# Kernel tuning notes

Hardware: AMD Instinct MI355X
Metric: run time of the kernel (lower is better)

Reference implementation:

```python
import jax, jax.numpy as jnp
import numpy as np

EMBED = 1024
HEADS = 16
HEAD_DIM = EMBED // HEADS


def setup_inputs() -> dict:
    key = jax.random.key(0)
    ks = jax.random.split(key, 11)
    B, S = 2, 2048
    scale = 1.0 / np.sqrt(EMBED)
    inp = {
        'Q': jax.random.normal(ks[0], (B, S, EMBED), jnp.float32),
        'K': jax.random.normal(ks[1], (B, S, EMBED), jnp.float32),
        'V': jax.random.normal(ks[2], (B, S, EMBED), jnp.float32),
        'Wq': jax.random.normal(ks[3], (EMBED, EMBED), jnp.float32) * scale,
        'bq': jnp.zeros((EMBED,), jnp.float32),
        'Wk': jax.random.normal(ks[4], (EMBED, EMBED), jnp.float32) * scale,
        'bk': jnp.zeros((EMBED,), jnp.float32),
        'Wv': jax.random.normal(ks[5], (EMBED, EMBED), jnp.float32) * scale,
        'bv': jnp.zeros((EMBED,), jnp.float32),
        'Wo': jax.random.normal(ks[6], (EMBED, EMBED), jnp.float32) * scale,
        'bo': jnp.zeros((EMBED,), jnp.float32),
    }
    return inp


def reference(Q, K, V, Wq, bq, Wk, bk, Wv, bv, Wo, bo):
    B, Sq, _ = Q.shape
    Sk = K.shape[1]
    # linear projections (torch nn.Linear: x @ W.T + b; here W stored as [in,out])
    q = Q @ Wq + bq
    k = K @ Wk + bk
    v = V @ Wv + bv
    # [B, H, S, D]
    q = q.reshape(B, Sq, HEADS, HEAD_DIM).transpose(0, 2, 1, 3)
    k = k.reshape(B, Sk, HEADS, HEAD_DIM).transpose(0, 2, 1, 3)
    v = v.reshape(B, Sk, HEADS, HEAD_DIM).transpose(0, 2, 1, 3)
    scores = jnp.einsum('bhqd,bhkd->bhqk', q, k) / jnp.sqrt(jnp.float32(HEAD_DIM))
    attn = jax.nn.softmax(scores, axis=-1)
    out = jnp.einsum('bhqk,bhkd->bhqd', attn, v)
    out = out.transpose(0, 2, 1, 3).reshape(B, Sq, EMBED)
    return out @ Wo + bo
```

## Files before the change

kernel.cpp:

```cpp
#include <hip/hip_runtime.h>

#define EMBED 1024
#define HEADS 16
#define HDIM  64
#define BATCH 2
#define SEQ   2048
#define MTOK  (BATCH*SEQ)

typedef _Float16 half_t;
typedef __attribute__((ext_vector_type(4))) float    f32x4;
typedef __attribute__((ext_vector_type(8))) _Float16 f16x8;
typedef __attribute__((ext_vector_type(4))) _Float16 f16x4;

#define MFMA16(a,b,c) __builtin_amdgcn_mfma_f32_16x16x32_f16(a,b,c,0,0,0)

#define GLOAD_LDS16(gp, lp)                                                     \
    __builtin_amdgcn_global_load_lds(                                           \
        (const __attribute__((address_space(1))) void*)(gp),                    \
        (__attribute__((address_space(3))) void*)(lp), 16, 0, 0)

#define QSCALE 0.18033688f

__global__ __launch_bounds__(256) void wt_kernel(const float* __restrict__ W0,
                                                 const float* __restrict__ W1,
                                                 const float* __restrict__ W2,
                                                 const float* __restrict__ W3,
                                                 half_t* __restrict__ T0,
                                                 half_t* __restrict__ T1,
                                                 half_t* __restrict__ T2,
                                                 half_t* __restrict__ T3)
{
    const int z = blockIdx.z;
    const float* W = (z == 0) ? W0 : (z == 1) ? W1 : (z == 2) ? W2 : W3;
    half_t* WT     = (z == 0) ? T0 : (z == 1) ? T1 : (z == 2) ? T2 : T3;

    __shared__ float tile[64][68];
    const int t  = threadIdx.x;
    const int n0 = blockIdx.x * 64;
    const int k0 = blockIdx.y * 64;
#pragma unroll
    for (int i = 0; i < 4; ++i) {
        int f = t + 256 * i;
        int r = f >> 4, c4 = (f & 15) << 2;
        float4 v = *(const float4*)(W + (size_t)(k0 + r) * EMBED + n0 + c4);
        tile[r][c4 + 0] = v.x; tile[r][c4 + 1] = v.y;
        tile[r][c4 + 2] = v.z; tile[r][c4 + 3] = v.w;
    }
    __syncthreads();
#pragma unroll
    for (int i = 0; i < 4; ++i) {
        int f = t + 256 * i;
        int nr = f >> 4, kc = (f & 15) << 2;
        f16x4 o;
        o[0] = (half_t)tile[kc + 0][nr];
        o[1] = (half_t)tile[kc + 1][nr];
        o[2] = (half_t)tile[kc + 2][nr];
        o[3] = (half_t)tile[kc + 3][nr];
        *(f16x4*)(WT + (size_t)(n0 + nr) * EMBED + k0 + kc) = o;
    }
}

__global__ __launch_bounds__(256, 3) void proj3_kernel(const float* __restrict__ Aq,
                                                       const float* __restrict__ Ak,
                                                       const float* __restrict__ Av,
                                                       const half_t* __restrict__ Btq,
                                                       const half_t* __restrict__ Btk,
                                                       const half_t* __restrict__ Btv,
                                                       const float*  __restrict__ bq,
                                                       const float*  __restrict__ bk,
                                                       const float*  __restrict__ bv,
                                                       half_t* __restrict__ oq,
                                                       half_t* __restrict__ ok,
                                                       half_t* __restrict__ ov)
{
    const int z = blockIdx.z;
    const float*  A    = (z == 0) ? Aq  : (z == 1) ? Ak  : Av;
    const half_t* Bt   = (z == 0) ? Btq : (z == 1) ? Btk : Btv;
    const float*  bias = (z == 0) ? bq  : (z == 1) ? bk  : bv;
    half_t*       out  = (z == 0) ? oq  : (z == 1) ? ok  : ov;

    __shared__ half_t As[128 * 64];
    __shared__ half_t Bs[128 * 64];
    const int tid = threadIdx.x, lane = tid & 63, g = lane >> 4, ln = lane & 15;
    const int w = tid >> 6, wm = w >> 1, wn = w & 1;
    const int m0 = blockIdx.x * 128, n0 = blockIdx.y * 128;
    const int srow8 = lane >> 3, schunk = lane & 7;

    f32x4 acc[4][4];
#pragma unroll
    for (int i = 0; i < 4; ++i)
#pragma unroll
        for (int j = 0; j < 4; ++j) acc[i][j] = (f32x4){0.f, 0.f, 0.f, 0.f};

    float4 v0[4], v1[4];
#pragma unroll
    for (int i = 0; i < 4; ++i) {
        int row = (i * 4 + w) * 8 + srow8;
        const float* src = A + (size_t)(m0 + row) * EMBED + schunk * 8;
        v0[i] = *(const float4*)(src);
        v1[i] = *(const float4*)(src + 4);
    }

    for (int kt = 0; kt < EMBED; kt += 64) {
#pragma unroll
        for (int i = 0; i < 4; ++i) {
            int row = (i * 4 + w) * 8 + srow8;
            GLOAD_LDS16(Bt + (size_t)(n0 + row) * EMBED + kt + schunk * 8,
                        (char*)Bs + (i * 4 + w) * 1024);
        }
#pragma unroll
        for (int i = 0; i < 4; ++i) {
            int row = (i * 4 + w) * 8 + srow8;
            f16x8 hv;
            hv[0] = (half_t)v0[i].x; hv[1] = (half_t)v0[i].y;
            hv[2] = (half_t)v0[i].z; hv[3] = (half_t)v0[i].w;
            hv[4] = (half_t)v1[i].x; hv[5] = (half_t)v1[i].y;
            hv[6] = (half_t)v1[i].z; hv[7] = (half_t)v1[i].w;
            *(f16x8*)(As + (size_t)row * 64 + schunk * 8) = hv;
        }
        __syncthreads();

        if (kt + 64 < EMBED) {
#pragma unroll
            for (int i = 0; i < 4; ++i) {
                int row = (i * 4 + w) * 8 + srow8;
                const float* src = A + (size_t)(m0 + row) * EMBED + kt + 64 + schunk * 8;
                v0[i] = *(const float4*)(src);
                v1[i] = *(const float4*)(src + 4);
            }
        }

#pragma unroll
        for (int k2 = 0; k2 < 2; ++k2) {
            f16x8 af[4], bf[4];
#pragma unroll
            for (int mi = 0; mi < 4; ++mi)
                af[mi] = *(const f16x8*)(As + (wm * 64 + mi * 16 + ln) * 64 + k2 * 32 + g * 8);
#pragma unroll
            for (int ni = 0; ni < 4; ++ni)
                bf[ni] = *(const f16x8*)(Bs + (wn * 64 + ni * 16 + ln) * 64 + k2 * 32 + g * 8);
#pragma unroll
            for (int mi = 0; mi < 4; ++mi)
#pragma unroll
                for (int ni = 0; ni < 4; ++ni)
                    acc[mi][ni] = MFMA16(af[mi], bf[ni], acc[mi][ni]);
        }
        __syncthreads();
    }

#pragma unroll
    for (int mi = 0; mi < 4; ++mi) {
#pragma unroll
        for (int ni = 0; ni < 4; ++ni) {
            int col = n0 + wn * 64 + ni * 16 + ln;
            float bb = bias[col];
            int h = col >> 6, d = col & 63;
            if (z == 2) {
                int row0 = m0 + wm * 64 + mi * 16 + g * 4;
                int b = row0 >> 11, s = row0 & 2047;
                f16x4 o4;
#pragma unroll
                for (int r = 0; r < 4; ++r)
                    o4[r] = (half_t)(acc[mi][ni][r] + bb);
                *(f16x4*)(out + ((size_t)(b * HEADS + h) * HDIM + d) * SEQ + s) = o4;
            } else {
#pragma unroll
                for (int r = 0; r < 4; ++r) {
                    int row = m0 + wm * 64 + mi * 16 + g * 4 + r;
                    int b = row >> 11, s = row & 2047;
                    float val = acc[mi][ni][r] + bb;
                    if (z == 0) val *= QSCALE;
                    out[((size_t)(b * HEADS + h) * SEQ + s) * HDIM + d] = (half_t)val;
                }
            }
        }
    }
}

__global__ __launch_bounds__(256, 4) void final_kernel(const half_t* __restrict__ A,
                                                       const half_t* __restrict__ Bt,
                                                       const float*  __restrict__ bias,
                                                       float* __restrict__ out)
{
    __shared__ half_t As[64 * 64];
    __shared__ half_t Bs[128 * 64];
    const int tid = threadIdx.x, lane = tid & 63, g = lane >> 4, ln = lane & 15;
    const int w = tid >> 6, wm = w >> 1, wn = w & 1;
    const int m0 = blockIdx.x * 64, n0 = blockIdx.y * 128;
    const int srow8 = lane >> 3, schunk = lane & 7;

    f32x4 acc[2][4];
#pragma unroll
    for (int i = 0; i < 2; ++i)
#pragma unroll
        for (int j = 0; j < 4; ++j) acc[i][j] = (f32x4){0.f, 0.f, 0.f, 0.f};

    for (int kt = 0; kt < EMBED; kt += 64) {
#pragma unroll
        for (int i = 0; i < 2; ++i) {
            int rg = i * 4 + w;
            GLOAD_LDS16(A + (size_t)(m0 + rg * 8 + srow8) * EMBED + kt + schunk * 8,
                        (char*)As + rg * 1024);
        }
#pragma unroll
        for (int i = 0; i < 4; ++i) {
            int rg = i * 4 + w;
            GLOAD_LDS16(Bt + (size_t)(n0 + rg * 8 + srow8) * EMBED + kt + schunk * 8,
                        (char*)Bs + rg * 1024);
        }
        __syncthreads();
#pragma unroll
        for (int k2 = 0; k2 < 2; ++k2) {
            f16x8 af[2], bf[4];
#pragma unroll
            for (int mi = 0; mi < 2; ++mi)
                af[mi] = *(const f16x8*)(As + (wm * 32 + mi * 16 + ln) * 64 + k2 * 32 + g * 8);
#pragma unroll
            for (int ni = 0; ni < 4; ++ni)
                bf[ni] = *(const f16x8*)(Bs + (wn * 64 + ni * 16 + ln) * 64 + k2 * 32 + g * 8);
#pragma unroll
            for (int mi = 0; mi < 2; ++mi)
#pragma unroll
                for (int ni = 0; ni < 4; ++ni)
                    acc[mi][ni] = MFMA16(af[mi], bf[ni], acc[mi][ni]);
        }
        __syncthreads();
    }
#pragma unroll
    for (int mi = 0; mi < 2; ++mi) {
#pragma unroll
        for (int ni = 0; ni < 4; ++ni) {
            int col = n0 + wn * 64 + ni * 16 + ln;
            float bb = bias[col];
#pragma unroll
            for (int r = 0; r < 4; ++r) {
                int row = m0 + wm * 32 + mi * 16 + g * 4 + r;
                out[(size_t)row * EMBED + col] = acc[mi][ni][r] + bb;
            }
        }
    }
}

__global__ __launch_bounds__(256, 2) void attn_kernel(const half_t* __restrict__ q,
                                                      const half_t* __restrict__ k,
                                                      const half_t* __restrict__ vt,
                                                      half_t* __restrict__ ao)
{
    __shared__ half_t Ks[64 * 64];
    __shared__ half_t Vs[64 * 64];
    __shared__ half_t Ps[4][32 * 72];
    const int tid = threadIdx.x, lane = tid & 63, g = lane >> 4, ln = lane & 15;
    const int w = tid >> 6;

    const int fid = blockIdx.x;
    const int j = fid & 7, t = fid >> 3;
    const int yhi = t >> 4, x = t & 15;
    const int bh = yhi * 8 + j;
    const int bb = bh >> 4, h = bh & 15;

    const half_t* qh = q  + (size_t)bh * SEQ * HDIM;
    const half_t* kh = k  + (size_t)bh * SEQ * HDIM;
    const half_t* vh = vt + (size_t)bh * HDIM * SEQ;
    const int qrow0 = x * 128 + w * 32;

    f16x8 qfrag[2][2];
#pragma unroll
    for (int mt = 0; mt < 2; ++mt)
#pragma unroll
        for (int kt = 0; kt < 2; ++kt)
            qfrag[mt][kt] = *(const f16x8*)(qh + (size_t)(qrow0 + mt * 16 + ln) * HDIM + kt * 32 + g * 8);

    f32x4 accO[2][4];
#pragma unroll
    for (int mt = 0; mt < 2; ++mt)
#pragma unroll
        for (int nt = 0; nt < 4; ++nt) accO[mt][nt] = (f32x4){0.f, 0.f, 0.f, 0.f};
    float lsum[2] = {0.f, 0.f};

    const int srow0 = tid >> 3;
    const int scol16 = tid & 7;

    {
        f16x8 rK[2], rV[2];
#pragma unroll
        for (int c = 0; c < 2; ++c) {
            int row = c * 32 + srow0;
            rK[c] = *(const f16x8*)(kh + (size_t)row * HDIM + scol16 * 8);
            rV[c] = *(const f16x8*)(vh + (size_t)row * SEQ + scol16 * 8);
        }
#pragma unroll
        for (int c = 0; c < 2; ++c) {
            int row = c * 32 + srow0;
            int off = row * 128 + ((scol16 * 16) ^ ((row & 7) << 4));
            *(f16x8*)((char*)Ks + off) = rK[c];
            *(f16x8*)((char*)Vs + off) = rV[c];
        }
    }
    __syncthreads();

    for (int kv = 0; kv < SEQ; kv += 64) {
        f32x4 accT[2][4];
#pragma unroll
        for (int mt = 0; mt < 2; ++mt)
#pragma unroll
            for (int kb = 0; kb < 4; ++kb) accT[mt][kb] = (f32x4){0.f, 0.f, 0.f, 0.f};
#pragma unroll
        for (int kt = 0; kt < 2; ++kt) {
            f16x8 kf[4];
#pragma unroll
            for (int kb = 0; kb < 4; ++kb) {
                int row = kb * 16 + ln;
                kf[kb] = *(const f16x8*)((char*)Ks + row * 128 + ((kt * 64 + g * 16) ^ ((row & 7) << 4)));
            }
            __builtin_amdgcn_s_setprio(1);
#pragma unroll
            for (int mt = 0; mt < 2; ++mt)
#pragma unroll
                for (int kb = 0; kb < 4; ++kb)
                    accT[mt][kb] = MFMA16(kf[kb], qfrag[mt][kt], accT[mt][kb]);
            __builtin_amdgcn_s_setprio(0);
        }

        const bool has_next = (kv + 64) < SEQ;
        f16x8 rK[2], rV[2];
        if (has_next) {
#pragma unroll
            for (int c = 0; c < 2; ++c) {
                int row = c * 32 + srow0;
                rK[c] = *(const f16x8*)(kh + (size_t)(kv + 64 + row) * HDIM + scol16 * 8);
                rV[c] = *(const f16x8*)(vh + (size_t)row * SEQ + kv + 64 + scol16 * 8);
            }
        }

#pragma unroll
        for (int mt = 0; mt < 2; ++mt) {
#pragma unroll
            for (int kb = 0; kb < 4; ++kb) {
                float p0 = __builtin_amdgcn_exp2f(accT[mt][kb][0]);
                float p1 = __builtin_amdgcn_exp2f(accT[mt][kb][1]);
                float p2 = __builtin_amdgcn_exp2f(accT[mt][kb][2]);
                float p3 = __builtin_amdgcn_exp2f(accT[mt][kb][3]);
                lsum[mt] += (p0 + p1) + (p2 + p3);
                f16x4 pv;
                pv[0] = (half_t)p0; pv[1] = (half_t)p1;
                pv[2] = (half_t)p2; pv[3] = (half_t)p3;
                *(f16x4*)(&Ps[w][(mt * 16 + ln) * 72 + kb * 16 + g * 4]) = pv;
            }
        }

#pragma unroll
        for (int kt = 0; kt < 2; ++kt) {
            f16x8 bf[4], ap[2];
#pragma unroll
            for (int nt = 0; nt < 4; ++nt) {
                int row = nt * 16 + ln;
                bf[nt] = *(const f16x8*)((char*)Vs + row * 128 + ((kt * 64 + g * 16) ^ ((row & 7) << 4)));
            }
#pragma unroll
            for (int mt = 0; mt < 2; ++mt)
                ap[mt] = *(const f16x8*)(&Ps[w][(mt * 16 + ln) * 72 + kt * 32 + g * 8]);
            __builtin_amdgcn_s_setprio(1);
#pragma unroll
            for (int mt = 0; mt < 2; ++mt)
#pragma unroll
                for (int nt = 0; nt < 4; ++nt)
                    accO[mt][nt] = MFMA16(ap[mt], bf[nt], accO[mt][nt]);
            __builtin_amdgcn_s_setprio(0);
        }

        if (has_next) {
            __syncthreads();
#pragma unroll
            for (int c = 0; c < 2; ++c) {
                int row = c * 32 + srow0;
                int off = row * 128 + ((scol16 * 16) ^ ((row & 7) << 4));
                *(f16x8*)((char*)Ks + off) = rK[c];
                *(f16x8*)((char*)Vs + off) = rV[c];
            }
            __syncthreads();
        }
    }

#pragma unroll
    for (int mt = 0; mt < 2; ++mt) {
        lsum[mt] += __shfl_xor(lsum[mt], 16);
        lsum[mt] += __shfl_xor(lsum[mt], 32);
    }

#pragma unroll
    for (int mt = 0; mt < 2; ++mt) {
#pragma unroll
        for (int r = 0; r < 4; ++r) {
            float linv = 1.0f / __shfl(lsum[mt], g * 4 + r);
            int srow_o = qrow0 + mt * 16 + g * 4 + r;
#pragma unroll
            for (int nt = 0; nt < 4; ++nt) {
                int d = nt * 16 + ln;
                ao[((size_t)(bb * SEQ + srow_o)) * EMBED + h * HDIM + d] =
                    (half_t)(accO[mt][nt][r] * linv);
            }
        }
    }
}

extern "C" void kernel_launch(void* const* d_in, const int* in_sizes, int n_in,
                              void* d_out, int out_size, void* d_ws, size_t ws_size,
                              hipStream_t stream)
{
    const float* Q  = (const float*)d_in[0];
    const float* K  = (const float*)d_in[1];
    const float* V  = (const float*)d_in[2];
    const float* Wq = (const float*)d_in[3];
    const float* bq = (const float*)d_in[4];
    const float* Wk = (const float*)d_in[5];
    const float* bk = (const float*)d_in[6];
    const float* Wv = (const float*)d_in[7];
    const float* bv = (const float*)d_in[8];
    const float* Wo = (const float*)d_in[9];
    const float* bo = (const float*)d_in[10];
    float* out = (float*)d_out;

    half_t* ws = (half_t*)d_ws;
    const size_t WSZ = (size_t)EMBED * EMBED;
    const size_t TSZ = (size_t)MTOK * EMBED;
    half_t* WqT = ws;
    half_t* WkT = WqT + WSZ;
    half_t* WvT = WkT + WSZ;
    half_t* WoT = WvT + WSZ;
    half_t* qf  = WoT + WSZ;
    half_t* kf  = qf + TSZ;
    half_t* vT  = kf + TSZ;
    half_t* ao  = vT + TSZ;

    dim3 blk(256);
    wt_kernel<<<dim3(16, 16, 4), blk, 0, stream>>>(Wq, Wk, Wv, Wo, WqT, WkT, WvT, WoT);

    proj3_kernel<<<dim3(MTOK / 128, EMBED / 128, 3), blk, 0, stream>>>(
        Q, K, V, WqT, WkT, WvT, bq, bk, bv, qf, kf, vT);

    attn_kernel<<<dim3(512), blk, 0, stream>>>(qf, kf, vT, ao);

    final_kernel<<<dim3(MTOK / 64, EMBED / 128), blk, 0, stream>>>(ao, WoT, bo, out);
}
```

Measured before the change: 118.4 us.

## Double-buffer weight tiles in LDS for projection and output GEMMs

Both the QKV projection GEMM and the output projection GEMM now keep two LDS buffers for the weight tile (and for the A tile in the final GEMM). The next k-tile is prefetched with global_load_lds while MFMAs run on the current one, hiding global load latency behind compute. This doubles LDS use per block, and the final kernel's launch-bounds occupancy hint drops from 4 to 3 blocks. Fewer resident blocks could offset the overlap gain.

```diff
diff --git a/kernel.cpp b/kernel.cpp
--- a/kernel.cpp
+++ b/kernel.cpp
@@ -80,7 +80,7 @@
     half_t*       out  = (z == 0) ? oq  : (z == 1) ? ok  : ov;
 
     __shared__ half_t As[128 * 64];
-    __shared__ half_t Bs[128 * 64];
+    __shared__ half_t Bs[2][128 * 64];
     const int tid = threadIdx.x, lane = tid & 63, g = lane >> 4, ln = lane & 15;
     const int w = tid >> 6, wm = w >> 1, wn = w & 1;
     const int m0 = blockIdx.x * 128, n0 = blockIdx.y * 128;
@@ -96,18 +96,17 @@
 #pragma unroll
     for (int i = 0; i < 4; ++i) {
         int row = (i * 4 + w) * 8 + srow8;
+        GLOAD_LDS16(Bt + (size_t)(n0 + row) * EMBED + schunk * 8,
+                    (char*)Bs[0] + (i * 4 + w) * 1024);
         const float* src = A + (size_t)(m0 + row) * EMBED + schunk * 8;
         v0[i] = *(const float4*)(src);
         v1[i] = *(const float4*)(src + 4);
     }
 
-    for (int kt = 0; kt < EMBED; kt += 64) {
-#pragma unroll
-        for (int i = 0; i < 4; ++i) {
-            int row = (i * 4 + w) * 8 + srow8;
-            GLOAD_LDS16(Bt + (size_t)(n0 + row) * EMBED + kt + schunk * 8,
-                        (char*)Bs + (i * 4 + w) * 1024);
-        }
+    for (int it = 0; it < 16; ++it) {
+        const int cur = it & 1;
+        const int kt = it * 64;
+
 #pragma unroll
         for (int i = 0; i < 4; ++i) {
             int row = (i * 4 + w) * 8 + srow8;
@@ -120,10 +119,12 @@
         }
         __syncthreads();
 
-        if (kt + 64 < EMBED) {
+        if (it + 1 < 16) {
 #pragma unroll
             for (int i = 0; i < 4; ++i) {
                 int row = (i * 4 + w) * 8 + srow8;
+                GLOAD_LDS16(Bt + (size_t)(n0 + row) * EMBED + kt + 64 + schunk * 8,
+                            (char*)Bs[cur ^ 1] + (i * 4 + w) * 1024);
                 const float* src = A + (size_t)(m0 + row) * EMBED + kt + 64 + schunk * 8;
                 v0[i] = *(const float4*)(src);
                 v1[i] = *(const float4*)(src + 4);
@@ -138,7 +139,7 @@
                 af[mi] = *(const f16x8*)(As + (wm * 64 + mi * 16 + ln) * 64 + k2 * 32 + g * 8);
 #pragma unroll
             for (int ni = 0; ni < 4; ++ni)
-                bf[ni] = *(const f16x8*)(Bs + (wn * 64 + ni * 16 + ln) * 64 + k2 * 32 + g * 8);
+                bf[ni] = *(const f16x8*)(Bs[cur] + (wn * 64 + ni * 16 + ln) * 64 + k2 * 32 + g * 8);
 #pragma unroll
             for (int mi = 0; mi < 4; ++mi)
 #pragma unroll
@@ -177,13 +178,13 @@
     }
 }
 
-__global__ __launch_bounds__(256, 4) void final_kernel(const half_t* __restrict__ A,
+__global__ __launch_bounds__(256, 3) void final_kernel(const half_t* __restrict__ A,
                                                        const half_t* __restrict__ Bt,
                                                        const float*  __restrict__ bias,
                                                        float* __restrict__ out)
 {
-    __shared__ half_t As[64 * 64];
-    __shared__ half_t Bs[128 * 64];
+    __shared__ half_t As[2][64 * 64];
+    __shared__ half_t Bs[2][128 * 64];
     const int tid = threadIdx.x, lane = tid & 63, g = lane >> 4, ln = lane & 15;
     const int w = tid >> 6, wm = w >> 1, wn = w & 1;
     const int m0 = blockIdx.x * 64, n0 = blockIdx.y * 128;
@@ -195,29 +196,48 @@
 #pragma unroll
         for (int j = 0; j < 4; ++j) acc[i][j] = (f32x4){0.f, 0.f, 0.f, 0.f};
 
-    for (int kt = 0; kt < EMBED; kt += 64) {
-#pragma unroll
-        for (int i = 0; i < 2; ++i) {
-            int rg = i * 4 + w;
-            GLOAD_LDS16(A + (size_t)(m0 + rg * 8 + srow8) * EMBED + kt + schunk * 8,
-                        (char*)As + rg * 1024);
-        }
-#pragma unroll
-        for (int i = 0; i < 4; ++i) {
-            int rg = i * 4 + w;
-            GLOAD_LDS16(Bt + (size_t)(n0 + rg * 8 + srow8) * EMBED + kt + schunk * 8,
-                        (char*)Bs + rg * 1024);
-        }
-        __syncthreads();
+#pragma unroll
+    for (int i = 0; i < 2; ++i) {
+        int rg = i * 4 + w;
+        GLOAD_LDS16(A + (size_t)(m0 + rg * 8 + srow8) * EMBED + schunk * 8,
+                    (char*)As[0] + rg * 1024);
+    }
+#pragma unroll
+    for (int i = 0; i < 4; ++i) {
+        int rg = i * 4 + w;
+        GLOAD_LDS16(Bt + (size_t)(n0 + rg * 8 + srow8) * EMBED + schunk * 8,
+                    (char*)Bs[0] + rg * 1024);
+    }
+    __syncthreads();
+
+    for (int it = 0; it < 16; ++it) {
+        const int cur = it & 1;
+        const int kt = it * 64;
+
+        if (it + 1 < 16) {
+#pragma unroll
+            for (int i = 0; i < 2; ++i) {
+                int rg = i * 4 + w;
+                GLOAD_LDS16(A + (size_t)(m0 + rg * 8 + srow8) * EMBED + kt + 64 + schunk * 8,
+                            (char*)As[cur ^ 1] + rg * 1024);
+            }
+#pragma unroll
+            for (int i = 0; i < 4; ++i) {
+                int rg = i * 4 + w;
+                GLOAD_LDS16(Bt + (size_t)(n0 + rg * 8 + srow8) * EMBED + kt + 64 + schunk * 8,
+                            (char*)Bs[cur ^ 1] + rg * 1024);
+            }
+        }
+
 #pragma unroll
         for (int k2 = 0; k2 < 2; ++k2) {
             f16x8 af[2], bf[4];
 #pragma unroll
             for (int mi = 0; mi < 2; ++mi)
-                af[mi] = *(const f16x8*)(As + (wm * 32 + mi * 16 + ln) * 64 + k2 * 32 + g * 8);
+                af[mi] = *(const f16x8*)(As[cur] + (wm * 32 + mi * 16 + ln) * 64 + k2 * 32 + g * 8);
 #pragma unroll
             for (int ni = 0; ni < 4; ++ni)
-                bf[ni] = *(const f16x8*)(Bs + (wn * 64 + ni * 16 + ln) * 64 + k2 * 32 + g * 8);
+                bf[ni] = *(const f16x8*)(Bs[cur] + (wn * 64 + ni * 16 + ln) * 64 + k2 * 32 + g * 8);
 #pragma unroll
             for (int mi = 0; mi < 2; ++mi)
 #pragma unroll
```

Result: no change. 120.4 us (+1.7%).
